# Optimization experiments

Measured on AMD Instinct MI355X. Metric: run time of the kernel, lower is better.

The kernel has to match this reference:

```python
import jax, jax.numpy as jnp
import numpy as np

N = 4096
IN_F = 256
OUT_F = 64
K = 4
ALPHA = 0.2  # LeakyReLU negative slope
NEG_INF = -9e15


def setup_inputs() -> dict:
    key = jax.random.key(0)
    k_h, k_w, k_a, k_e, k_m = jax.random.split(key, 5)
    h = jax.random.normal(k_h, (N, IN_F), dtype=jnp.float32)
    # xavier_uniform with gain=1.414
    def xavier(k, shape, gain=1.414):
        fan_in, fan_out = shape[0], shape[1]
        limit = gain * np.sqrt(6.0 / (fan_in + fan_out))
        return jax.random.uniform(k, shape, jnp.float32, -limit, limit)
    W = xavier(k_w, (IN_F, OUT_F))
    a = xavier(k_a, (2 * OUT_F, 1))
    vals = jax.random.uniform(k_e, (K, N, N), dtype=jnp.float32)
    mask = jax.random.uniform(k_m, (K, N, N), dtype=jnp.float32) < 0.05
    edge_attr = jnp.where(mask, vals, 0.0)
    return {"h": h, "edge_attr": edge_attr, "W": W, "a": a}


def reference(h, edge_attr, W, a):
    # h: [N, IN_F], edge_attr: [K, N, N], W: [IN_F, OUT_F], a: [2*OUT_F, 1]
    Wh = h @ W                                   # [N, OUT_F]
    Wh1 = Wh @ a[:OUT_F, :]                      # [N, 1]
    Wh2 = Wh @ a[OUT_F:, :]                      # [N, 1]
    e = jax.nn.leaky_relu(Wh1 + Wh2.T, negative_slope=ALPHA)  # [N, N]
    e = e[None, :, :] * edge_attr                # [K, N, N]
    e = jnp.where(edge_attr > 0, e, NEG_INF)
    att = jax.nn.softmax(e, axis=1)              # softmax over dim=1, as in torch
    # dropout is identity in eval mode
    # batched replacement for the per-channel python loop of matmuls
    hp = jnp.einsum('kij,jf->kif', att, Wh)      # [K, N, OUT_F]
    out = jnp.transpose(hp, (1, 0, 2)).reshape(N, K * OUT_F)  # concat dim=1
    return jax.nn.elu(out), att
```

## Files before the change

kernel.cpp:

```cpp
#include <hip/hip_runtime.h>

#define NN 4096
#define IN_F 256
#define OUT_F 64
#define K_CH 4
#define ALPHA 0.2f
#define ROWS1 32
#define IC1 128
#define BSTRIDE 264

typedef __bf16 bf16;
typedef __attribute__((ext_vector_type(8))) __bf16 bf16x8;
typedef __attribute__((ext_vector_type(4))) __bf16 bf16x4;
typedef __attribute__((ext_vector_type(4))) float f32x4;

__global__ __launch_bounds__(256) void k0_wh(const float* __restrict__ h,
                                             const float* __restrict__ W,
                                             const float* __restrict__ a,
                                             float* __restrict__ Wh,
                                             float* __restrict__ Wh1,
                                             float* __restrict__ Wh2) {
    int tid = threadIdx.x;
    int wave = tid >> 6, lane = tid & 63;
    int i = blockIdx.x * 4 + wave;
    const float* hrow = h + (size_t)i * IN_F;
    float acc = 0.f;
    #pragma unroll 8
    for (int c = 0; c < IN_F; ++c)
        acc += hrow[c] * W[c * OUT_F + lane];
    Wh[(size_t)i * OUT_F + lane] = acc;
    float v1 = acc * a[lane];
    float v2 = acc * a[OUT_F + lane];
    #pragma unroll
    for (int o = 32; o > 0; o >>= 1) {
        v1 += __shfl_xor(v1, o, 64);
        v2 += __shfl_xor(v2, o, 64);
    }
    if (lane == 0) { Wh1[i] = v1; Wh2[i] = v2; }
}

__global__ __launch_bounds__(256) void k0_transpose(const float* __restrict__ Wh,
                                                    bf16* __restrict__ WhT) {
    __shared__ float lds[OUT_F * 65];
    int tid = threadIdx.x;
    int i0 = blockIdx.x * 64;
    int f = tid & 63;
    int r0 = tid >> 6;
    #pragma unroll
    for (int s = 0; s < 16; ++s) {
        int r = r0 * 16 + s;
        lds[f * 65 + r] = Wh[(size_t)(i0 + r) * OUT_F + f];
    }
    __syncthreads();
    int f2 = tid >> 2;
    int c0 = (tid & 3) * 16;
    bf16x8 v0, v1;
    #pragma unroll
    for (int s = 0; s < 8; ++s) {
        v0[s] = (bf16)lds[f2 * 65 + c0 + s];
        v1[s] = (bf16)lds[f2 * 65 + c0 + 8 + s];
    }
    *(bf16x8*)&WhT[(size_t)f2 * NN + i0 + c0] = v0;
    *(bf16x8*)&WhT[(size_t)f2 * NN + i0 + c0 + 8] = v1;
}

__global__ __launch_bounds__(256) void k1_colsum(const float* __restrict__ edge,
                                                 const float* __restrict__ Wh1,
                                                 const float* __restrict__ Wh2,
                                                 float* __restrict__ partial) {
    int tid = threadIdx.x;
    int kch = blockIdx.z;
    int j0 = blockIdx.y * 1024 + tid * 4;
    int ic = blockIdx.x;
    int ibase = ic * ROWS1;
    f32x4 w2 = *(const f32x4*)&Wh2[j0];
    f32x4 w1v[ROWS1 / 4];
    #pragma unroll
    for (int t = 0; t < ROWS1 / 4; ++t)
        w1v[t] = *(const f32x4*)&Wh1[ibase + t * 4];
    f32x4 s = {0.f, 0.f, 0.f, 0.f};
    const float* base = edge + ((size_t)kch * NN + ibase) * NN + j0;
    f32x4 r[8];
    #pragma unroll
    for (int t = 0; t < 8; ++t)
        r[t] = *(const f32x4*)(base + (size_t)t * NN);
    #pragma unroll
    for (int ii = 0; ii < ROWS1; ++ii) {
        f32x4 e = r[ii & 7];
        if (ii + 8 < ROWS1)
            r[ii & 7] = *(const f32x4*)(base + (size_t)(ii + 8) * NN);
        float wh1 = w1v[ii >> 2][ii & 3];
        #pragma unroll
        for (int c = 0; c < 4; ++c) {
            float xv = wh1 + w2[c];
            float lk = xv > 0.f ? xv : ALPHA * xv;
            float val = e[c] > 0.f ? __expf(lk * e[c]) : 0.f;
            bf16 vb = (bf16)val;
            s[c] += (float)vb;
        }
    }
    *(f32x4*)(partial + ((size_t)kch * IC1 + ic) * NN + j0) = s;
}

__global__ __launch_bounds__(256) void k1_reduce(const float* __restrict__ partial,
                                                 const bf16* __restrict__ WhT,
                                                 float* __restrict__ s_inv,
                                                 bf16* __restrict__ WhTs) {
    __shared__ float red[256];
    __shared__ float inv_l[64];
    int tid = threadIdx.x;
    int kch = blockIdx.y;
    int jl = tid & 63, g = tid >> 6;
    int jbase = blockIdx.x * 64;
    int j = jbase + jl;
    const float* pb = partial + (size_t)kch * IC1 * NN;
    float s = 0.f;
    #pragma unroll 8
    for (int t = 0; t < IC1 / 4; ++t)
        s += pb[(size_t)(g * (IC1 / 4) + t) * NN + j];
    red[tid] = s;
    __syncthreads();
    if (tid < 64) {
        float tot = red[tid] + red[tid + 64] + red[tid + 128] + red[tid + 192];
        float iv = tot > 0.f ? 1.f / tot : 0.f;
        s_inv[kch * NN + j] = iv;
        inv_l[tid] = iv;
    }
    __syncthreads();
    int f = tid >> 2;
    int c0 = (tid & 3) * 16;
    bf16x8 a0 = *(const bf16x8*)&WhT[(size_t)f * NN + jbase + c0];
    bf16x8 a1 = *(const bf16x8*)&WhT[(size_t)f * NN + jbase + c0 + 8];
    bf16x8 o0, o1;
    #pragma unroll
    for (int s2 = 0; s2 < 8; ++s2) {
        o0[s2] = (bf16)((float)a0[s2] * inv_l[c0 + s2]);
        o1[s2] = (bf16)((float)a1[s2] * inv_l[c0 + 8 + s2]);
    }
    bf16* wb = WhTs + ((size_t)kch * OUT_F + f) * NN + jbase + c0;
    *(bf16x8*)wb = o0;
    *(bf16x8*)(wb + 8) = o1;
}

__global__ __launch_bounds__(256, 4) void k2_fused(const float* __restrict__ edge,
                                                   const float* __restrict__ Wh1,
                                                   const float* __restrict__ Wh2,
                                                   const float* __restrict__ s_inv,
                                                   const bf16* __restrict__ WhTs,
                                                   float* __restrict__ att_out,
                                                   float* __restrict__ hp_part) {
    __shared__ bf16 ldsB[OUT_F * BSTRIDE];
    int tid = threadIdx.x;
    int itile = blockIdx.x;
    int jq = blockIdx.y;
    int kch = blockIdx.z;
    int wave = tid >> 6, lane = tid & 63;
    int n16 = lane & 15, quad = lane >> 4;
    int i_row = itile * 64 + wave * 16 + n16;
    int jbase = jq * 1024;
    const float* erow = edge + ((size_t)kch * NN + i_row) * NN + jbase + quad * 8;
    float* arow = att_out + ((size_t)kch * NN + i_row) * NN + jbase + quad * 8;
    const float* w2p = Wh2 + jbase + quad * 8;
    const float* ivp = s_inv + kch * NN + jbase + quad * 8;
    float wh1 = Wh1[i_row];
    f32x4 acc[4] = {};
    f32x4 pf0[4], pf1[4];
    #pragma unroll
    for (int t = 0; t < 4; ++t) {
        pf0[t] = *(const f32x4*)(erow + t * 32);
        pf1[t] = *(const f32x4*)(erow + t * 32 + 4);
    }
    int f = tid >> 2, part = (tid & 3) * 64;
    const bf16* wsrc = WhTs + ((size_t)kch * OUT_F + f) * NN + jbase + part;
    #pragma unroll
    for (int slab = 0; slab < 4; ++slab) {
        __syncthreads();
        #pragma unroll
        for (int u = 0; u < 8; ++u) {
            bf16x8 v = *(const bf16x8*)(wsrc + slab * 256 + u * 8);
            *(bf16x8*)&ldsB[f * BSTRIDE + part + u * 8] = v;
        }
        __syncthreads();
        #pragma unroll
        for (int t = 0; t < 8; ++t) {
            int g = slab * 8 + t;
            int cur = g & 3;
            f32x4 e0 = pf0[cur], e1 = pf1[cur];
            if (g + 4 < 32) {
                pf0[cur] = *(const f32x4*)(erow + (g + 4) * 32);
                pf1[cur] = *(const f32x4*)(erow + (g + 4) * 32 + 4);
            }
            f32x4 w2a = *(const f32x4*)(w2p + g * 32);
            f32x4 w2b = *(const f32x4*)(w2p + g * 32 + 4);
            f32x4 iva = *(const f32x4*)(ivp + g * 32);
            f32x4 ivb = *(const f32x4*)(ivp + g * 32 + 4);
            bf16x8 afrag;
            f32x4 av0, av1;
            #pragma unroll
            for (int c = 0; c < 8; ++c) {
                float e  = c < 4 ? e0[c]  : e1[c - 4];
                float wv = c < 4 ? w2a[c] : w2b[c - 4];
                float iv = c < 4 ? iva[c] : ivb[c - 4];
                float xv = wh1 + wv;
                float lk = xv > 0.f ? xv : ALPHA * xv;
                float val = e > 0.f ? __expf(lk * e) : 0.f;
                bf16 vb = (bf16)val;
                afrag[c] = vb;
                float attv = (float)vb * iv;
                if (c < 4) av0[c] = attv; else av1[c - 4] = attv;
            }
            *(f32x4*)(arow + g * 32) = av0;
            *(f32x4*)(arow + g * 32 + 4) = av1;
            int jl = t * 32 + quad * 8;
            #pragma unroll
            for (int ft = 0; ft < 4; ++ft) {
                bf16x8 bfrag = *(const bf16x8*)&ldsB[(ft * 16 + n16) * BSTRIDE + jl];
                acc[ft] = __builtin_amdgcn_mfma_f32_16x16x32_bf16(afrag, bfrag, acc[ft], 0, 0, 0);
            }
        }
    }
    float* hb = hp_part + (((size_t)kch * 4 + jq) * NN) * OUT_F;
    #pragma unroll
    for (int ft = 0; ft < 4; ++ft) {
        #pragma unroll
        for (int r = 0; r < 4; ++r) {
            int i_g = itile * 64 + wave * 16 + quad * 4 + r;
            hb[(size_t)i_g * OUT_F + ft * 16 + n16] = acc[ft][r];
        }
    }
}

__global__ __launch_bounds__(256) void k3_elu(const float* __restrict__ hp_part,
                                              float* __restrict__ out) {
    int i = blockIdx.x;
    int tid = threadIdx.x;
    int kch = tid >> 6, f = tid & 63;
    float s = 0.f;
    #pragma unroll
    for (int jq = 0; jq < 4; ++jq)
        s += hp_part[(((size_t)kch * 4 + jq) * NN + i) * OUT_F + f];
    out[(size_t)i * (K_CH * OUT_F) + tid] = s > 0.f ? s : __expf(s) - 1.f;
}

extern "C" void kernel_launch(void* const* d_in, const int* in_sizes, int n_in,
                              void* d_out, int out_size, void* d_ws, size_t ws_size,
                              hipStream_t stream) {
    (void)out_size; (void)ws_size;
    const float *h = nullptr, *edge = nullptr, *W = nullptr, *a = nullptr;
    for (int i = 0; i < n_in; ++i) {
        int sz = in_sizes[i];
        if (sz == NN * IN_F)               h    = (const float*)d_in[i];
        else if (sz == K_CH * NN * NN)     edge = (const float*)d_in[i];
        else if (sz == IN_F * OUT_F)       W    = (const float*)d_in[i];
        else if (sz == 2 * OUT_F)          a    = (const float*)d_in[i];
    }

    char* ws = (char*)d_ws;
    size_t off = 0;
    float* Wh      = (float*)(ws + off); off += (size_t)NN * OUT_F * 4;
    float* Wh1     = (float*)(ws + off); off += NN * 4;
    float* Wh2     = (float*)(ws + off); off += NN * 4;
    float* s_inv   = (float*)(ws + off); off += (size_t)K_CH * NN * 4;
    bf16*  WhT     = (bf16*) (ws + off); off += (size_t)OUT_F * NN * 2;
    bf16*  WhTs    = (bf16*) (ws + off); off += (size_t)K_CH * OUT_F * NN * 2;
    float* partial = (float*)(ws + off); off += (size_t)K_CH * IC1 * NN * 4;
    float* hp_part = (float*)(ws + off); off += (size_t)K_CH * 4 * NN * OUT_F * 4;

    float* out_h   = (float*)d_out;
    float* att_out = out_h + (size_t)NN * (K_CH * OUT_F);

    k0_wh<<<dim3(NN / 4), 256, 0, stream>>>(h, W, a, Wh, Wh1, Wh2);
    k0_transpose<<<dim3(NN / 64), 256, 0, stream>>>(Wh, WhT);
    k1_colsum<<<dim3(IC1, 4, K_CH), 256, 0, stream>>>(edge, Wh1, Wh2, partial);
    k1_reduce<<<dim3(NN / 64, K_CH), 256, 0, stream>>>(partial, WhT, s_inv, WhTs);
    k2_fused<<<dim3(64, 4, K_CH), 256, 0, stream>>>(edge, Wh1, Wh2, s_inv, WhTs,
                                                    att_out, hp_part);
    k3_elu<<<dim3(NN), 256, 0, stream>>>(hp_part, out_h);
}
```

Baseline: 579.8 us.

## Cache bf16 exp values from colsum pass and reuse them in fused attention kernel

The column-sum kernel now writes the unnormalized bf16 exp(leaky(e)*edge) values into a workspace buffer and uses nontemporal loads for the edge tensor. The fused kernel reads this bf16 buffer instead of re-reading the fp32 edge tensor, dropping the recomputation of leaky-relu and exp. This replaces a second fp32 edge read with a bf16 write plus a bf16 read, so total memory traffic stays about the same while compute in the fused kernel drops. It also needs a large extra workspace allocation.

After: 555.8 us. -4.1%, faster.

```diff
diff --git a/kernel.cpp b/kernel.cpp
--- a/kernel.cpp
+++ b/kernel.cpp
@@ -67,6 +67,7 @@
 __global__ __launch_bounds__(256) void k1_colsum(const float* __restrict__ edge,
                                                  const float* __restrict__ Wh1,
                                                  const float* __restrict__ Wh2,
+                                                 bf16* __restrict__ p_buf,
                                                  float* __restrict__ partial) {
     int tid = threadIdx.x;
     int kch = blockIdx.z;
@@ -80,24 +81,29 @@
         w1v[t] = *(const f32x4*)&Wh1[ibase + t * 4];
     f32x4 s = {0.f, 0.f, 0.f, 0.f};
     const float* base = edge + ((size_t)kch * NN + ibase) * NN + j0;
+    bf16* pbase = p_buf + ((size_t)kch * NN + ibase) * NN + j0;
     f32x4 r[8];
     #pragma unroll
     for (int t = 0; t < 8; ++t)
-        r[t] = *(const f32x4*)(base + (size_t)t * NN);
+        r[t] = __builtin_nontemporal_load((const f32x4*)(base + (size_t)t * NN));
     #pragma unroll
     for (int ii = 0; ii < ROWS1; ++ii) {
         f32x4 e = r[ii & 7];
         if (ii + 8 < ROWS1)
-            r[ii & 7] = *(const f32x4*)(base + (size_t)(ii + 8) * NN);
+            r[ii & 7] = __builtin_nontemporal_load(
+                            (const f32x4*)(base + (size_t)(ii + 8) * NN));
         float wh1 = w1v[ii >> 2][ii & 3];
+        bf16x4 pv;
         #pragma unroll
         for (int c = 0; c < 4; ++c) {
             float xv = wh1 + w2[c];
             float lk = xv > 0.f ? xv : ALPHA * xv;
             float val = e[c] > 0.f ? __expf(lk * e[c]) : 0.f;
             bf16 vb = (bf16)val;
+            pv[c] = vb;
             s[c] += (float)vb;
         }
+        *(bf16x4*)(pbase + (size_t)ii * NN) = pv;
     }
     *(f32x4*)(partial + ((size_t)kch * IC1 + ic) * NN + j0) = s;
 }
@@ -142,9 +148,7 @@
     *(bf16x8*)(wb + 8) = o1;
 }
 
-__global__ __launch_bounds__(256, 4) void k2_fused(const float* __restrict__ edge,
-                                                   const float* __restrict__ Wh1,
-                                                   const float* __restrict__ Wh2,
+__global__ __launch_bounds__(256, 4) void k2_fused(const bf16* __restrict__ p_buf,
                                                    const float* __restrict__ s_inv,
                                                    const bf16* __restrict__ WhTs,
                                                    float* __restrict__ att_out,
@@ -158,18 +162,14 @@
     int n16 = lane & 15, quad = lane >> 4;
     int i_row = itile * 64 + wave * 16 + n16;
     int jbase = jq * 1024;
-    const float* erow = edge + ((size_t)kch * NN + i_row) * NN + jbase + quad * 8;
+    const bf16* prow = p_buf + ((size_t)kch * NN + i_row) * NN + jbase + quad * 8;
     float* arow = att_out + ((size_t)kch * NN + i_row) * NN + jbase + quad * 8;
-    const float* w2p = Wh2 + jbase + quad * 8;
     const float* ivp = s_inv + kch * NN + jbase + quad * 8;
-    float wh1 = Wh1[i_row];
     f32x4 acc[4] = {};
-    f32x4 pf0[4], pf1[4];
-    #pragma unroll
-    for (int t = 0; t < 4; ++t) {
-        pf0[t] = *(const f32x4*)(erow + t * 32);
-        pf1[t] = *(const f32x4*)(erow + t * 32 + 4);
-    }
+    bf16x8 pf[8];
+    #pragma unroll
+    for (int t = 0; t < 8; ++t)
+        pf[t] = *(const bf16x8*)(prow + t * 32);
     int f = tid >> 2, part = (tid & 3) * 64;
     const bf16* wsrc = WhTs + ((size_t)kch * OUT_F + f) * NN + jbase + part;
     #pragma unroll
@@ -184,30 +184,16 @@
         #pragma unroll
         for (int t = 0; t < 8; ++t) {
             int g = slab * 8 + t;
-            int cur = g & 3;
-            f32x4 e0 = pf0[cur], e1 = pf1[cur];
-            if (g + 4 < 32) {
-                pf0[cur] = *(const f32x4*)(erow + (g + 4) * 32);
-                pf1[cur] = *(const f32x4*)(erow + (g + 4) * 32 + 4);
-            }
-            f32x4 w2a = *(const f32x4*)(w2p + g * 32);
-            f32x4 w2b = *(const f32x4*)(w2p + g * 32 + 4);
+            bf16x8 pv = pf[g & 7];
+            if (g + 8 < 32)
+                pf[g & 7] = *(const bf16x8*)(prow + (g + 8) * 32);
             f32x4 iva = *(const f32x4*)(ivp + g * 32);
             f32x4 ivb = *(const f32x4*)(ivp + g * 32 + 4);
-            bf16x8 afrag;
             f32x4 av0, av1;
             #pragma unroll
-            for (int c = 0; c < 8; ++c) {
-                float e  = c < 4 ? e0[c]  : e1[c - 4];
-                float wv = c < 4 ? w2a[c] : w2b[c - 4];
-                float iv = c < 4 ? iva[c] : ivb[c - 4];
-                float xv = wh1 + wv;
-                float lk = xv > 0.f ? xv : ALPHA * xv;
-                float val = e > 0.f ? __expf(lk * e) : 0.f;
-                bf16 vb = (bf16)val;
-                afrag[c] = vb;
-                float attv = (float)vb * iv;
-                if (c < 4) av0[c] = attv; else av1[c - 4] = attv;
+            for (int c = 0; c < 4; ++c) {
+                av0[c] = (float)pv[c] * iva[c];
+                av1[c] = (float)pv[c + 4] * ivb[c];
             }
             *(f32x4*)(arow + g * 32) = av0;
             *(f32x4*)(arow + g * 32 + 4) = av1;
@@ -215,7 +201,7 @@
             #pragma unroll
             for (int ft = 0; ft < 4; ++ft) {
                 bf16x8 bfrag = *(const bf16x8*)&ldsB[(ft * 16 + n16) * BSTRIDE + jl];
-                acc[ft] = __builtin_amdgcn_mfma_f32_16x16x32_bf16(afrag, bfrag, acc[ft], 0, 0, 0);
+                acc[ft] = __builtin_amdgcn_mfma_f32_16x16x32_bf16(pv, bfrag, acc[ft], 0, 0, 0);
             }
         }
     }
@@ -265,15 +251,15 @@
     bf16*  WhTs    = (bf16*) (ws + off); off += (size_t)K_CH * OUT_F * NN * 2;
     float* partial = (float*)(ws + off); off += (size_t)K_CH * IC1 * NN * 4;
     float* hp_part = (float*)(ws + off); off += (size_t)K_CH * 4 * NN * OUT_F * 4;
+    bf16*  p_buf   = (bf16*) (ws + off); off += (size_t)K_CH * NN * NN * 2;
 
     float* out_h   = (float*)d_out;
     float* att_out = out_h + (size_t)NN * (K_CH * OUT_F);
 
     k0_wh<<<dim3(NN / 4), 256, 0, stream>>>(h, W, a, Wh, Wh1, Wh2);
     k0_transpose<<<dim3(NN / 64), 256, 0, stream>>>(Wh, WhT);
-    k1_colsum<<<dim3(IC1, 4, K_CH), 256, 0, stream>>>(edge, Wh1, Wh2, partial);
+    k1_colsum<<<dim3(IC1, 4, K_CH), 256, 0, stream>>>(edge, Wh1, Wh2, p_buf, partial);
     k1_reduce<<<dim3(NN / 64, K_CH), 256, 0, stream>>>(partial, WhT, s_inv, WhTs);
-    k2_fused<<<dim3(64, 4, K_CH), 256, 0, stream>>>(edge, Wh1, Wh2, s_inv, WhTs,
-                                                    att_out, hp_part);
+    k2_fused<<<dim3(64, 4, K_CH), 256, 0, stream>>>(p_buf, s_inv, WhTs, att_out, hp_part);
     k3_elu<<<dim3(NN), 256, 0, stream>>>(hp_part, out_h);
 }
```
